# Kernel tuning notes

Hardware: AMD Instinct MI355X
Metric: run time of the kernel (lower is better)

Reference implementation:

```python
import jax, jax.numpy as jnp
import numpy as np

N = 50000      # nodes in batched graph
E = 800000     # homomorphism mappings per kernel (avg 16/node)
D_IN = 128     # input node feature dim
D_K = 64       # per-kernel output dim (3 kernels -> concat 192)
D_H = 192      # hom_conv_dim per layer
B = 64         # graphs in batch
A_HID = 10     # final agg output dim


def setup_inputs() -> dict:
    key = jax.random.key(0)
    ks = jax.random.split(key, 24)
    s = 0.05
    inp = {
        "x": jax.random.normal(ks[0], (N, D_IN), jnp.float32),
        "map00": jax.random.randint(ks[1], (2, E), 0, N),
        "map01": jax.random.randint(ks[2], (2, E), 0, N),
        "map02": jax.random.randint(ks[3], (2, E), 0, N),
        "map10": jax.random.randint(ks[4], (2, E), 0, N),
        "map11": jax.random.randint(ks[5], (2, E), 0, N),
        "map12": jax.random.randint(ks[6], (2, E), 0, N),
        "batch_idx": jnp.sort(jax.random.randint(ks[7], (N,), 0, B)),
        "batch_size": B,
        # layer 0 kernel weights (in D_IN)
        "W00": jax.random.normal(ks[8], (D_IN, D_K), jnp.float32) * s,
        "b00": jnp.zeros((D_K,), jnp.float32),
        "W01": jax.random.normal(ks[9], (D_IN, D_K), jnp.float32) * s,
        "b01": jnp.zeros((D_K,), jnp.float32),
        "W02": jax.random.normal(ks[10], (D_IN, D_K), jnp.float32) * s,
        "b02": jnp.zeros((D_K,), jnp.float32),
        # layer 1 kernel weights (in D_H = 192)
        "W10": jax.random.normal(ks[11], (D_H, D_K), jnp.float32) * s,
        "b10": jnp.zeros((D_K,), jnp.float32),
        "W11": jax.random.normal(ks[12], (D_H, D_K), jnp.float32) * s,
        "b11": jnp.zeros((D_K,), jnp.float32),
        "W12": jax.random.normal(ks[13], (D_H, D_K), jnp.float32) * s,
        "b12": jnp.zeros((D_K,), jnp.float32),
        # agg MLP: Linear(192,256) + ReLU + Linear(256,10)
        "A1": jax.random.normal(ks[14], (D_H, 256), jnp.float32) * s,
        "ba1": jnp.zeros((256,), jnp.float32),
        "A2": jax.random.normal(ks[15], (256, A_HID), jnp.float32) * s,
        "ba2": jnp.zeros((A_HID,), jnp.float32),
    }
    return inp


def _kernel(feat, W, b, mapping):
    # hom-kernel: linear transform, gather images, scatter_add to roots, relu
    h = feat @ W + b                                  # [N, d_k]
    msg = h[mapping[1]]                               # gather  [E, d_k]
    agg = jax.ops.segment_sum(msg, mapping[0], num_segments=feat.shape[0])
    return jax.nn.relu(agg)                           # [N, d_k]


def reference(x, map00, map01, map02, map10, map11, map12, batch_idx,
              batch_size, W00, b00, W01, b01, W02, b02,
              W10, b10, W11, b11, W12, b12, A1, ba1, A2, ba2):
    # layer 0: three hom-kernels, concat along feature dim
    f = jnp.concatenate([
        _kernel(x, W00, b00, map00),
        _kernel(x, W01, b01, map01),
        _kernel(x, W02, b02, map02)], axis=1)          # [N, 192]
    # layer 1
    f = jnp.concatenate([
        _kernel(f, W10, b10, map10),
        _kernel(f, W11, b11, map11),
        _kernel(f, W12, b12, map12)], axis=1)          # [N, 192]
    # batch pooling via scatter_add (sum per graph)
    pooled = jax.ops.segment_sum(f, batch_idx, num_segments=batch_size)  # [B, 192]
    # agg MLP
    h = jax.nn.relu(pooled @ A1 + ba1) @ A2 + ba2      # [B, 10]
    return h
```

## Files before the change

kernel.cpp:

```cpp
#include <hip/hip_runtime.h>
#include <hip/hip_bf16.h>


#define CAPSB 9216
#define CAPCOL 12800
#define CHUNK 4096
#define PTHREADS 512
#define EPT 8
#define SBSHIFT 9
#define POOLROWS 32

typedef __attribute__((ext_vector_type(8))) short bf16x8;
typedef __attribute__((ext_vector_type(4))) float f32x4;

__device__ inline unsigned short f2bf(float x) {
    union { float f; unsigned u; } c; c.f = x;
    unsigned r = (c.u + 0x7FFFu + ((c.u >> 16) & 1u)) >> 16;
    return (unsigned short)r;
}
__device__ inline float bf2f(unsigned u16) {
    union { unsigned u; float f; } c; c.u = (u16 & 0xffffu) << 16; return c.f;
}
__device__ inline float lo16f(unsigned v) {
    union { unsigned u; float f; } c; c.u = v << 16; return c.f;
}
__device__ inline float hi16f(unsigned v) {
    union { unsigned u; float f; } c; c.u = v & 0xffff0000u; return c.f;
}

__global__ void prepack_w(const float* __restrict__ W0, const float* __restrict__ W1,
                          const float* __restrict__ W2, const float* __restrict__ W3,
                          const float* __restrict__ W4, const float* __restrict__ W5,
                          unsigned short* __restrict__ wp,
                          unsigned short* __restrict__ h, int N,
                          int* __restrict__ cnt, int NSB,
                          float* __restrict__ pooled) {
    const int m = blockIdx.x;
    if (m == 6) {
        for (int i = threadIdx.x; i < 192; i += 256) h[(size_t)N * 192 + i] = 0;
        for (int i = threadIdx.x; i < 6 * NSB; i += 256) cnt[i] = 0;
        for (int i = threadIdx.x; i < 64 * 192; i += 256) pooled[i] = 0.f;
        return;
    }
    const float* W = (m == 0) ? W0 : (m == 1) ? W1 : (m == 2) ? W2
                   : (m == 3) ? W3 : (m == 4) ? W4 : W5;
    const int K = (m < 3) ? 128 : 192;
    unsigned short* o = wp + (size_t)m * 12288;
    for (int idx = threadIdx.x; idx < K * 64; idx += 256) {
        int k = idx >> 6, col = idx & 63;
        o[((k >> 3) * 64 + col) * 8 + (k & 7)] = f2bf(W[idx]);
    }
}

template <int INBF16>
__global__ void gemm_mfma(const void* __restrict__ in_, int M, int K,
                          const unsigned short* __restrict__ wpack,
                          const float* __restrict__ b0, const float* __restrict__ b1,
                          const float* __restrict__ b2, int mslot,
                          unsigned short* __restrict__ h) {
    __shared__ __align__(16) unsigned short Ws[12288];
    __shared__ __align__(16) unsigned short As[2048];

    const int g = blockIdx.y;
    const float* bias = (g == 0) ? b0 : ((g == 1) ? b1 : b2);
    const unsigned short* wp = wpack + (size_t)(mslot + g) * 12288;

    const int t = threadIdx.x;
    for (int i = t; i < K * 32; i += 256)
        ((int*)Ws)[i] = ((const int*)wp)[i];

    const int m0   = blockIdx.x * 64;
    const int lane = t & 63;
    const int wrow = (t >> 6) * 16;

    const int arow = t >> 2;
    const int aseg = t & 3;
    const int aswz = arow * 32 + ((aseg ^ ((arow >> 1) & 3)) << 3);
    const int grow = m0 + arow;

    const float*          ainf = (const float*)in_ + (size_t)grow * K + aseg * 8;
    const unsigned short* ainb = (const unsigned short*)in_ + (size_t)grow * K + aseg * 8;

    const int lrow = wrow + (lane & 15);
    const int aoff = lrow * 32 + ((((lane >> 4)) ^ ((lrow >> 1) & 3)) << 3);
    const int kq   = lane >> 4;

    f32x4 acc[4] = {};

    const int nsteps = K >> 5;
    for (int s = 0; s < nsteps; ++s) {
        __syncthreads();
        bf16x8 av = {};
        if (grow < M) {
            if (INBF16) {
                av = *reinterpret_cast<const bf16x8*>(ainb + s * 32);
            } else {
                float4 v0 = *reinterpret_cast<const float4*>(ainf + s * 32);
                float4 v1 = *reinterpret_cast<const float4*>(ainf + s * 32 + 4);
                av[0] = (short)f2bf(v0.x); av[1] = (short)f2bf(v0.y);
                av[2] = (short)f2bf(v0.z); av[3] = (short)f2bf(v0.w);
                av[4] = (short)f2bf(v1.x); av[5] = (short)f2bf(v1.y);
                av[6] = (short)f2bf(v1.z); av[7] = (short)f2bf(v1.w);
            }
        }
        *reinterpret_cast<bf16x8*>(&As[aswz]) = av;
        __syncthreads();

        bf16x8 af = *reinterpret_cast<const bf16x8*>(&As[aoff]);
        const int kg = s * 4 + kq;
        #pragma unroll
        for (int n = 0; n < 4; ++n) {
            bf16x8 bfv = *reinterpret_cast<const bf16x8*>(
                &Ws[(size_t)(kg * 64 + n * 16 + (lane & 15)) * 8]);
            acc[n] = __builtin_amdgcn_mfma_f32_16x16x32_bf16(af, bfv, acc[n], 0, 0, 0);
        }
    }

    #pragma unroll
    for (int n = 0; n < 4; ++n) {
        int col = n * 16 + (lane & 15);
        float bv = bias[col];
        #pragma unroll
        for (int r = 0; r < 4; ++r) {
            int row = m0 + wrow + (lane >> 4) * 4 + r;
            if (row < M)
                h[(size_t)row * 192 + g * 64 + col] = f2bf(acc[n][r] + bv);
        }
    }
}

__global__ void part_coarse(const int* __restrict__ m0, const int* __restrict__ m1,
                            const int* __restrict__ m2, const int* __restrict__ m3,
                            const int* __restrict__ m4, const int* __restrict__ m5,
                            int E, int NSB, int* __restrict__ cnt,
                            unsigned* __restrict__ p1) {
    const int m = blockIdx.y;
    const int* mp = (m == 0) ? m0 : (m == 1) ? m1 : (m == 2) ? m2
                  : (m == 3) ? m3 : (m == 4) ? m4 : m5;
    __shared__ int hist[128];
    __shared__ int scanb[128];
    __shared__ int loff[128];
    __shared__ int delta[128];
    __shared__ unsigned stage[CHUNK];
    const int c0 = blockIdx.x * CHUNK;
    const int t = threadIdx.x;

    int d[EPT]; unsigned srcs[EPT];
    #pragma unroll
    for (int k = 0; k < EPT; ++k) {
        int e = c0 + k * PTHREADS + t;
        bool v = e < E;
        d[k]    = v ? mp[e] : -1;
        srcs[k] = v ? (unsigned)mp[E + e] : 0u;
    }

    if (t < 128) hist[t] = 0;
    __syncthreads();
    #pragma unroll
    for (int k = 0; k < EPT; ++k)
        if (d[k] >= 0) atomicAdd(&hist[d[k] >> SBSHIFT], 1);
    __syncthreads();

    if (t < 128) scanb[t] = hist[t];
    __syncthreads();
    for (int off = 1; off < 128; off <<= 1) {
        int v = (t < 128 && t >= off) ? scanb[t - off] : 0;
        __syncthreads();
        if (t < 128) scanb[t] += v;
        __syncthreads();
    }
    if (t < NSB) {
        int c = hist[t];
        int lstart = scanb[t] - c;
        int gbase = (c > 0) ? atomicAdd(&cnt[m * NSB + t], c) : 0;
        loff[t]  = lstart;
        delta[t] = (m * NSB + t) * CAPSB + gbase - lstart;
    }
    __syncthreads();

    #pragma unroll
    for (int k = 0; k < EPT; ++k) {
        if (d[k] >= 0) {
            int sb = d[k] >> SBSHIFT;
            int pos = atomicAdd(&loff[sb], 1);
            stage[pos] = (srcs[k] << 16) | (unsigned)d[k];
        }
    }
    __syncthreads();

    const int total = scanb[127];
    for (int i = t; i < total; i += PTHREADS) {
        unsigned r = stage[i];
        int sb = (r & 0xffffu) >> SBSHIFT;
        int gidx = delta[sb] + i;
        if (gidx - (m * NSB + sb) * CAPSB < CAPSB)
            p1[gidx] = r;
    }
}

__global__ void sb_sort(int NSB, int N, const int* __restrict__ cnt,
                        const unsigned* __restrict__ p1,
                        unsigned* __restrict__ cols, int* __restrict__ rows) {
    const int sb = blockIdx.x;
    const int m  = blockIdx.y;
    __shared__ unsigned rec[CAPSB];
    __shared__ int bin[512];
    __shared__ int pend[512];
    __shared__ int scanbuf[512];
    const int t = threadIdx.x;
    const size_t basep = (size_t)(m * NSB + sb) * CAPSB;
    const size_t basec = (size_t)(m * NSB + sb) * CAPCOL;
    const int c = min(cnt[m * NSB + sb], CAPSB);

    for (int i = t; i < c; i += 512) rec[i] = p1[basep + i];
    bin[t] = 0;
    __syncthreads();
    for (int i = t; i < c; i += 512)
        atomicAdd(&bin[rec[i] & 511], 1);
    __syncthreads();

    int b0 = bin[t];
    int p0 = (b0 + 7) & ~7;
    scanbuf[t] = p0;
    __syncthreads();
    for (int off = 1; off < 512; off <<= 1) {
        int v = (t >= off) ? scanbuf[t - off] : 0;
        __syncthreads();
        scanbuf[t] += v;
        __syncthreads();
    }
    int excl = scanbuf[t] - p0;
    bin[t]  = excl;
    pend[t] = excl + p0;
    __syncthreads();

    {
        int n = (sb << SBSHIFT) + t;
        if (n < N) rows[(size_t)m * N + n] = (int)(basec + pend[t]);
    }
    __syncthreads();

    for (int i = t; i < c; i += 512) {
        unsigned r = rec[i];
        int pos = atomicAdd(&bin[r & 511], 1);
        cols[basec + pos] = (r >> 16) * 384u;
    }
    __syncthreads();

    const unsigned dummy = (unsigned)N * 384u;
    for (int k = bin[t]; k < pend[t]; ++k)
        cols[basec + k] = dummy;
}

__device__ inline void aggG(const char* __restrict__ hb,
                            const unsigned* __restrict__ cols,
                            int i, float& ax, float& ay) {
    uint4 ca = *reinterpret_cast<const uint4*>(cols + i);
    unsigned v0 = *reinterpret_cast<const unsigned*>(hb + ca.x);
    unsigned v1 = *reinterpret_cast<const unsigned*>(hb + ca.y);
    unsigned v2 = *reinterpret_cast<const unsigned*>(hb + ca.z);
    unsigned v3 = *reinterpret_cast<const unsigned*>(hb + ca.w);
    ax += (lo16f(v0) + lo16f(v1)) + (lo16f(v2) + lo16f(v3));
    ay += (hi16f(v0) + hi16f(v1)) + (hi16f(v2) + hi16f(v3));
}

__global__ void csr_agg(const unsigned short* __restrict__ h, const int* __restrict__ rows,
                        const unsigned* __restrict__ cols, int N, int NSB, int mapBase,
                        unsigned short* __restrict__ f) {
    const int g = blockIdx.y;
    const int m = mapBase + g;
    const int lane = threadIdx.x & 63;
    const int half4 = (lane >> 5) << 2;
    const int fp = (lane & 31) * 2;
    const int wid = (blockIdx.x * blockDim.x + threadIdx.x) >> 6;
    const int n0 = wid * 2;
    const int n1 = n0 + 1;
    if (n0 >= N) return;
    const bool has1 = (n1 < N);

    const size_t base0 = (size_t)(m * NSB + (n0 >> SBSHIFT)) * CAPCOL;
    int s0 = ((n0 & 511) == 0) ? (int)base0 : rows[(size_t)m * N + n0 - 1];
    int e0 = rows[(size_t)m * N + n0];
    int s1 = 0, e1 = 0;
    if (has1) {
        s1 = e0;
        e1 = rows[(size_t)m * N + n1];
    }
    const char* hb = (const char*)(h + g * 64 + fp);

    float ax0 = 0.f, ay0 = 0.f, ax1 = 0.f, ay1 = 0.f;
    int i0 = s0 + half4, i1 = s1 + half4;
    const int f0 = e0 - 16 + half4, f1 = e1 - 16 + half4;

    while (i0 <= f0 && i1 <= f1) {
        uint4 ca = *reinterpret_cast<const uint4*>(cols + i0);
        uint4 cb = *reinterpret_cast<const uint4*>(cols + i0 + 8);
        uint4 cc = *reinterpret_cast<const uint4*>(cols + i1);
        uint4 cd = *reinterpret_cast<const uint4*>(cols + i1 + 8);
        unsigned va0 = *reinterpret_cast<const unsigned*>(hb + ca.x);
        unsigned va1 = *reinterpret_cast<const unsigned*>(hb + ca.y);
        unsigned va2 = *reinterpret_cast<const unsigned*>(hb + ca.z);
        unsigned va3 = *reinterpret_cast<const unsigned*>(hb + ca.w);
        unsigned vb0 = *reinterpret_cast<const unsigned*>(hb + cb.x);
        unsigned vb1 = *reinterpret_cast<const unsigned*>(hb + cb.y);
        unsigned vb2 = *reinterpret_cast<const unsigned*>(hb + cb.z);
        unsigned vb3 = *reinterpret_cast<const unsigned*>(hb + cb.w);
        unsigned vc0 = *reinterpret_cast<const unsigned*>(hb + cc.x);
        unsigned vc1 = *reinterpret_cast<const unsigned*>(hb + cc.y);
        unsigned vc2 = *reinterpret_cast<const unsigned*>(hb + cc.z);
        unsigned vc3 = *reinterpret_cast<const unsigned*>(hb + cc.w);
        unsigned vd0 = *reinterpret_cast<const unsigned*>(hb + cd.x);
        unsigned vd1 = *reinterpret_cast<const unsigned*>(hb + cd.y);
        unsigned vd2 = *reinterpret_cast<const unsigned*>(hb + cd.z);
        unsigned vd3 = *reinterpret_cast<const unsigned*>(hb + cd.w);
        ax0 += ((lo16f(va0) + lo16f(va1)) + (lo16f(va2) + lo16f(va3)))
             + ((lo16f(vb0) + lo16f(vb1)) + (lo16f(vb2) + lo16f(vb3)));
        ay0 += ((hi16f(va0) + hi16f(va1)) + (hi16f(va2) + hi16f(va3)))
             + ((hi16f(vb0) + hi16f(vb1)) + (hi16f(vb2) + hi16f(vb3)));
        ax1 += ((lo16f(vc0) + lo16f(vc1)) + (lo16f(vc2) + lo16f(vc3)))
             + ((lo16f(vd0) + lo16f(vd1)) + (lo16f(vd2) + lo16f(vd3)));
        ay1 += ((hi16f(vc0) + hi16f(vc1)) + (hi16f(vc2) + hi16f(vc3)))
             + ((hi16f(vd0) + hi16f(vd1)) + (hi16f(vd2) + hi16f(vd3)));
        i0 += 16; i1 += 16;
    }
    while (i0 <= f0) { aggG(hb, cols, i0, ax0, ay0); aggG(hb, cols, i0 + 8, ax0, ay0); i0 += 16; }
    while (i1 <= f1) { aggG(hb, cols, i1, ax1, ay1); aggG(hb, cols, i1 + 8, ax1, ay1); i1 += 16; }
    if (i0 < e0) aggG(hb, cols, i0, ax0, ay0);
    if (i1 < e1) aggG(hb, cols, i1, ax1, ay1);

    ax0 += __shfl_xor(ax0, 32); ay0 += __shfl_xor(ay0, 32);
    ax1 += __shfl_xor(ax1, 32); ay1 += __shfl_xor(ay1, 32);
    if (half4 == 0) {
        unsigned pk0 = (unsigned)f2bf(fmaxf(ax0, 0.f)) | ((unsigned)f2bf(fmaxf(ay0, 0.f)) << 16);
        *reinterpret_cast<unsigned*>(f + (size_t)n0 * 192 + g * 64 + fp) = pk0;
        if (has1) {
            unsigned pk1 = (unsigned)f2bf(fmaxf(ax1, 0.f)) | ((unsigned)f2bf(fmaxf(ay1, 0.f)) << 16);
            *reinterpret_cast<unsigned*>(f + (size_t)n1 * 192 + g * 64 + fp) = pk1;
        }
    }
}

__global__ void pool_kernel(const unsigned short* __restrict__ f, const int* __restrict__ bidx,
                            int N, float* __restrict__ pooled) {
    const int c  = threadIdx.x;
    const int r0 = blockIdx.x * POOLROWS;
    const int r1 = min(r0 + POOLROWS, N);
    if (r0 >= N) return;
    float acc = 0.f;
    int cur = bidx[r0];
    for (int r = r0; r < r1; ++r) {
        int b = bidx[r];
        if (b != cur) {
            atomicAdd(&pooled[(size_t)cur * 192 + c], acc);
            acc = 0.f;
            cur = b;
        }
        acc += bf2f(f[(size_t)r * 192 + c]);
    }
    atomicAdd(&pooled[(size_t)cur * 192 + c], acc);
}

__global__ void mlp_kernel(const float* __restrict__ pooled,
                           const float* __restrict__ A1, const float* __restrict__ ba1,
                           const float* __restrict__ A2, const float* __restrict__ ba2,
                           float* __restrict__ out) {
    __shared__ float p[192];
    __shared__ float hid[256];
    const int b = blockIdx.x;
    const int t = threadIdx.x;
    if (t < 192) p[t] = pooled[(size_t)b * 192 + t];
    __syncthreads();
    float acc = ba1[t];
    for (int k = 0; k < 192; ++k) acc += p[k] * A1[(size_t)k * 256 + t];
    hid[t] = fmaxf(acc, 0.f);
    __syncthreads();
    if (t < 10) {
        float o = ba2[t];
        for (int k = 0; k < 256; ++k) o += hid[k] * A2[(size_t)k * 10 + t];
        out[(size_t)b * 10 + t] = o;
    }
}

extern "C" void kernel_launch(void* const* d_in, const int* in_sizes, int n_in,
                              void* d_out, int out_size, void* d_ws, size_t ws_size,
                              hipStream_t stream) {
    const float* x      = (const float*)d_in[0];
    const int*   map00  = (const int*)d_in[1];
    const int*   map01  = (const int*)d_in[2];
    const int*   map02  = (const int*)d_in[3];
    const int*   map10  = (const int*)d_in[4];
    const int*   map11  = (const int*)d_in[5];
    const int*   map12  = (const int*)d_in[6];
    const int*   bidx   = (const int*)d_in[7];
    const float* W00 = (const float*)d_in[9];  const float* b00 = (const float*)d_in[10];
    const float* W01 = (const float*)d_in[11]; const float* b01 = (const float*)d_in[12];
    const float* W02 = (const float*)d_in[13]; const float* b02 = (const float*)d_in[14];
    const float* W10 = (const float*)d_in[15]; const float* b10 = (const float*)d_in[16];
    const float* W11 = (const float*)d_in[17]; const float* b11 = (const float*)d_in[18];
    const float* W12 = (const float*)d_in[19]; const float* b12 = (const float*)d_in[20];
    const float* A1  = (const float*)d_in[21]; const float* ba1 = (const float*)d_in[22];
    const float* A2  = (const float*)d_in[23]; const float* ba2 = (const float*)d_in[24];

    const int N   = in_sizes[0] / 128;
    const int E   = in_sizes[1] / 2;
    const int NSB = (N + 511) >> SBSHIFT;

    unsigned short* bufH = (unsigned short*)d_ws;
    unsigned short* bufF = bufH + (size_t)(N + 1) * 192;
    float*    pooled = (float*)(bufF + (size_t)N * 192);
    int*      cnt    = (int*)(pooled + 64 * 192);
    unsigned* p1     = (unsigned*)(cnt + 6 * NSB);
    unsigned* cols   = p1 + (size_t)6 * NSB * CAPSB;
    int*      rows   = (int*)(cols + (size_t)6 * NSB * CAPCOL + 16);
    unsigned short* wpack = (unsigned short*)(rows + (size_t)6 * N);

    dim3 gemmGrid((N + 63) / 64, 3);
    dim3 p1Grid((E + CHUNK - 1) / CHUNK, 6);
    dim3 sortGrid(NSB, 6);
    dim3 aggGrid((N + 7) / 8, 3);

    prepack_w<<<7, 256, 0, stream>>>(W00, W01, W02, W10, W11, W12, wpack,
                                     bufH, N, cnt, NSB, pooled);
    part_coarse<<<p1Grid, PTHREADS, 0, stream>>>(map00, map01, map02,
                                                 map10, map11, map12,
                                                 E, NSB, cnt, p1);
    sb_sort<<<sortGrid, PTHREADS, 0, stream>>>(NSB, N, cnt, p1, cols, rows);
    gemm_mfma<0><<<gemmGrid, 256, 0, stream>>>(x, N, 128, wpack, b00, b01, b02, 0, bufH);
    csr_agg<<<aggGrid, 256, 0, stream>>>(bufH, rows, cols, N, NSB, 0, bufF);
    gemm_mfma<1><<<gemmGrid, 256, 0, stream>>>(bufF, N, 192, wpack, b10, b11, b12, 3, bufH);
    csr_agg<<<aggGrid, 256, 0, stream>>>(bufH, rows, cols, N, NSB, 3, bufF);
    pool_kernel<<<(N + POOLROWS - 1) / POOLROWS, 192, 0, stream>>>(bufF, bidx, N, pooled);
    mlp_kernel<<<64, 256, 0, stream>>>(pooled, A1, ba1, A2, ba2, (float*)d_out);
}
```

Baseline: 209.7 us.

## Fuse three kernel GEMMs per block and stream weights per K-step; widen sort blocks

The GEMM now has each block compute all three 64-column kernel outputs, so the A tile is loaded and converted once instead of three times. Weight slices are staged into a smaller shared buffer on every K-step rather than loading the whole packed weight up front. This cuts input reads to a third but adds a global weight load each step and triples the accumulator registers per thread. Separately, the superblock sort launches 1024 threads and guards the 512-entry histogram and scan logic so only half the threads take part in it.

```diff
diff --git a/kernel.cpp b/kernel.cpp
--- a/kernel.cpp
+++ b/kernel.cpp
@@ -58,17 +58,10 @@
                           const float* __restrict__ b0, const float* __restrict__ b1,
                           const float* __restrict__ b2, int mslot,
                           unsigned short* __restrict__ h) {
-    __shared__ __align__(16) unsigned short Ws[12288];
+    __shared__ __align__(16) unsigned short Ws[6144];
     __shared__ __align__(16) unsigned short As[2048];
 
-    const int g = blockIdx.y;
-    const float* bias = (g == 0) ? b0 : ((g == 1) ? b1 : b2);
-    const unsigned short* wp = wpack + (size_t)(mslot + g) * 12288;
-
     const int t = threadIdx.x;
-    for (int i = t; i < K * 32; i += 256)
-        ((int*)Ws)[i] = ((const int*)wp)[i];
-
     const int m0   = blockIdx.x * 64;
     const int lane = t & 63;
     const int wrow = (t >> 6) * 16;
@@ -85,7 +78,11 @@
     const int aoff = lrow * 32 + ((((lane >> 4)) ^ ((lrow >> 1) & 3)) << 3);
     const int kq   = lane >> 4;
 
-    f32x4 acc[4] = {};
+    const int* wsrc0 = (const int*)(wpack + (size_t)(mslot + 0) * 12288);
+    const int* wsrc1 = (const int*)(wpack + (size_t)(mslot + 1) * 12288);
+    const int* wsrc2 = (const int*)(wpack + (size_t)(mslot + 2) * 12288);
+
+    f32x4 acc[3][4] = {};
 
     const int nsteps = K >> 5;
     for (int s = 0; s < nsteps; ++s) {
@@ -104,27 +101,48 @@
             }
         }
         *reinterpret_cast<bf16x8*>(&As[aswz]) = av;
+        {
+            int i0 = s * 1024 + t;
+            ((int*)Ws)[t]        = wsrc0[i0];
+            ((int*)Ws)[t + 256]  = wsrc0[i0 + 256];
+            ((int*)Ws)[t + 512]  = wsrc0[i0 + 512];
+            ((int*)Ws)[t + 768]  = wsrc0[i0 + 768];
+            ((int*)Ws)[t + 1024] = wsrc1[i0];
+            ((int*)Ws)[t + 1280] = wsrc1[i0 + 256];
+            ((int*)Ws)[t + 1536] = wsrc1[i0 + 512];
+            ((int*)Ws)[t + 1792] = wsrc1[i0 + 768];
+            ((int*)Ws)[t + 2048] = wsrc2[i0];
+            ((int*)Ws)[t + 2304] = wsrc2[i0 + 256];
+            ((int*)Ws)[t + 2560] = wsrc2[i0 + 512];
+            ((int*)Ws)[t + 2816] = wsrc2[i0 + 768];
+        }
         __syncthreads();
 
         bf16x8 af = *reinterpret_cast<const bf16x8*>(&As[aoff]);
-        const int kg = s * 4 + kq;
+        #pragma unroll
+        for (int g = 0; g < 3; ++g) {
+            #pragma unroll
+            for (int n = 0; n < 4; ++n) {
+                bf16x8 bfv = *reinterpret_cast<const bf16x8*>(
+                    &Ws[(size_t)((g * 4 + kq) * 64 + n * 16 + (lane & 15)) * 8]);
+                acc[g][n] = __builtin_amdgcn_mfma_f32_16x16x32_bf16(af, bfv, acc[g][n], 0, 0, 0);
+            }
+        }
+    }
+
+    #pragma unroll
+    for (int g = 0; g < 3; ++g) {
+        const float* bias = (g == 0) ? b0 : ((g == 1) ? b1 : b2);
         #pragma unroll
         for (int n = 0; n < 4; ++n) {
-            bf16x8 bfv = *reinterpret_cast<const bf16x8*>(
-                &Ws[(size_t)(kg * 64 + n * 16 + (lane & 15)) * 8]);
-            acc[n] = __builtin_amdgcn_mfma_f32_16x16x32_bf16(af, bfv, acc[n], 0, 0, 0);
-        }
-    }
-
-    #pragma unroll
-    for (int n = 0; n < 4; ++n) {
-        int col = n * 16 + (lane & 15);
-        float bv = bias[col];
-        #pragma unroll
-        for (int r = 0; r < 4; ++r) {
-            int row = m0 + wrow + (lane >> 4) * 4 + r;
-            if (row < M)
-                h[(size_t)row * 192 + g * 64 + col] = f2bf(acc[n][r] + bv);
+            int col = n * 16 + (lane & 15);
+            float bv = bias[col];
+            #pragma unroll
+            for (int r = 0; r < 4; ++r) {
+                int row = m0 + wrow + (lane >> 4) * 4 + r;
+                if (row < M)
+                    h[(size_t)row * 192 + g * 64 + col] = f2bf(acc[g][n][r] + bv);
+            }
         }
     }
 }
@@ -212,44 +230,43 @@
     const size_t basec = (size_t)(m * NSB + sb) * CAPCOL;
     const int c = min(cnt[m * NSB + sb], CAPSB);
 
-    for (int i = t; i < c; i += 512) rec[i] = p1[basep + i];
-    bin[t] = 0;
-    __syncthreads();
-    for (int i = t; i < c; i += 512)
+    for (int i = t; i < c; i += 1024) rec[i] = p1[basep + i];
+    if (t < 512) bin[t] = 0;
+    __syncthreads();
+    for (int i = t; i < c; i += 1024)
         atomicAdd(&bin[rec[i] & 511], 1);
     __syncthreads();
 
-    int b0 = bin[t];
-    int p0 = (b0 + 7) & ~7;
-    scanbuf[t] = p0;
+    int p0 = 0;
+    if (t < 512) { int b0 = bin[t]; p0 = (b0 + 7) & ~7; scanbuf[t] = p0; }
     __syncthreads();
     for (int off = 1; off < 512; off <<= 1) {
-        int v = (t >= off) ? scanbuf[t - off] : 0;
-        __syncthreads();
-        scanbuf[t] += v;
-        __syncthreads();
-    }
-    int excl = scanbuf[t] - p0;
-    bin[t]  = excl;
-    pend[t] = excl + p0;
-    __syncthreads();
-
-    {
+        int v = (t < 512 && t >= off) ? scanbuf[t - off] : 0;
+        __syncthreads();
+        if (t < 512) scanbuf[t] += v;
+        __syncthreads();
+    }
+    if (t < 512) {
+        int excl = scanbuf[t] - p0;
+        bin[t]  = excl;
+        pend[t] = excl + p0;
         int n = (sb << SBSHIFT) + t;
         if (n < N) rows[(size_t)m * N + n] = (int)(basec + pend[t]);
     }
     __syncthreads();
 
-    for (int i = t; i < c; i += 512) {
+    for (int i = t; i < c; i += 1024) {
         unsigned r = rec[i];
         int pos = atomicAdd(&bin[r & 511], 1);
         cols[basec + pos] = (r >> 16) * 384u;
     }
     __syncthreads();
 
-    const unsigned dummy = (unsigned)N * 384u;
-    for (int k = bin[t]; k < pend[t]; ++k)
-        cols[basec + k] = dummy;
+    if (t < 512) {
+        const unsigned dummy = (unsigned)N * 384u;
+        for (int k = bin[t]; k < pend[t]; ++k)
+            cols[basec + k] = dummy;
+    }
 }
 
 __device__ inline void aggG(const char* __restrict__ hb,
@@ -414,7 +431,7 @@
     int*      rows   = (int*)(cols + (size_t)6 * NSB * CAPCOL + 16);
     unsigned short* wpack = (unsigned short*)(rows + (size_t)6 * N);
 
-    dim3 gemmGrid((N + 63) / 64, 3);
+    dim3 gemmGrid((N + 63) / 64);
     dim3 p1Grid((E + CHUNK - 1) / CHUNK, 6);
     dim3 sortGrid(NSB, 6);
     dim3 aggGrid((N + 7) / 8, 3);
@@ -424,7 +441,7 @@
     part_coarse<<<p1Grid, PTHREADS, 0, stream>>>(map00, map01, map02,
                                                  map10, map11, map12,
                                                  E, NSB, cnt, p1);
-    sb_sort<<<sortGrid, PTHREADS, 0, stream>>>(NSB, N, cnt, p1, cols, rows);
+    sb_sort<<<sortGrid, 1024, 0, stream>>>(NSB, N, cnt, p1, cols, rows);
     gemm_mfma<0><<<gemmGrid, 256, 0, stream>>>(x, N, 128, wpack, b00, b01, b02, 0, bufH);
     csr_agg<<<aggGrid, 256, 0, stream>>>(bufH, rows, cols, N, NSB, 0, bufF);
     gemm_mfma<1><<<gemmGrid, 256, 0, stream>>>(bufF, N, 192, wpack, b10, b11, b12, 3, bufH);
```

Result: no change. 206.5 us (-1.5%).
